# Kernel tuning notes

Hardware: AMD Instinct MI355X
Metric: run time of the kernel (lower is better)

Reference implementation:

```python
import jax, jax.numpy as jnp
import numpy as np

N_NODES = 100000
N_EDGES = 1600000
N_GRAPHS = 256
NEG_SLOPE_GAT = 0.2   # GATConv default
NEG_SLOPE_ACT = 0.01  # F.leaky_relu default


def _leaky(x, s):
    return jnp.where(x >= 0, x, s * x)


def _gat_layer(x, src, dst, W, a_src, a_dst, b, n):
    # h = W x ; per-node attention logits
    h = x @ W                      # [N, D]
    al_s = h @ a_src               # [N]
    al_d = h @ a_dst               # [N]
    e = _leaky(al_s[src] + al_d[dst], NEG_SLOPE_GAT)  # [E]
    # segment softmax over incoming edges of each dst node
    m = jax.ops.segment_max(e, dst, num_segments=n)
    m = jnp.where(jnp.isfinite(m), m, 0.0)
    ex = jnp.exp(e - m[dst])
    s = jax.ops.segment_sum(ex, dst, num_segments=n)
    alpha = ex / (s[dst] + 1e-16)
    out = jax.ops.segment_sum(h[src] * alpha[:, None], dst, num_segments=n)
    return out + b


def setup_inputs() -> dict:
    key = jax.random.key(0)
    ks = jax.random.split(key, 12)
    x = jax.random.normal(ks[0], (N_NODES, 72), dtype=jnp.float32)
    edge_index = jax.random.randint(ks[1], (2, N_EDGES), 0, N_NODES, dtype=jnp.int64)
    batch = jnp.sort(jax.random.randint(ks[2], (N_NODES,), 0, N_GRAPHS, dtype=jnp.int64))
    def glorot(k, shape):
        fan = shape[0] + shape[-1]
        return jax.random.normal(k, shape, dtype=jnp.float32) * jnp.sqrt(2.0 / fan)
    return {
        "x": x, "edge_index": edge_index, "batch": batch,
        "W1": glorot(ks[3], (72, 64)),
        "a_src1": glorot(ks[4], (64,)), "a_dst1": glorot(ks[5], (64,)),
        "b1": jnp.zeros((64,), jnp.float32),
        "W2": glorot(ks[6], (64, 64)),
        "a_src2": glorot(ks[7], (64,)), "a_dst2": glorot(ks[8], (64,)),
        "b2": jnp.zeros((64,), jnp.float32),
        "fcW": glorot(ks[9], (64, 2)),
        "fcb": jnp.zeros((2,), jnp.float32),
    }


def reference(x, edge_index, batch, W1, a_src1, a_dst1, b1, W2, a_src2, a_dst2, b2, fcW, fcb):
    n = x.shape[0]
    # PyG GATConv adds self-loops by default
    loops = jnp.arange(n, dtype=edge_index.dtype)
    src = jnp.concatenate([edge_index[0], loops])
    dst = jnp.concatenate([edge_index[1], loops])
    h = _gat_layer(x, src, dst, W1, a_src1, a_dst1, b1, n)
    h = _leaky(h, NEG_SLOPE_ACT)
    h = _gat_layer(h, src, dst, W2, a_src2, a_dst2, b2, n)
    # global mean pool over graphs
    sums = jax.ops.segment_sum(h, batch, num_segments=N_GRAPHS)
    cnt = jax.ops.segment_sum(jnp.ones((n,), h.dtype), batch, num_segments=N_GRAPHS)
    pooled = sums / jnp.maximum(cnt, 1.0)[:, None]
    # dropout is identity at inference
    return pooled @ fcW + fcb
```

## Files before the change

### kernel.cpp

```cpp
#include <hip/hip_runtime.h>
#include <hip/hip_bf16.h>
#include <math.h>


#define NPB 256
#define EPB 4096
#define PSTRIDE 4608
#define XPAD 68

__device__ __forceinline__ unsigned int f2bf(float v) {
    unsigned int b = __float_as_uint(v);
    b += 0x7FFFu + ((b >> 16) & 1u);
    return b >> 16;
}

__global__ __launch_bounds__(256) void init_all(int* __restrict__ bcur, int NB) {
    int i = blockIdx.x * 256 + threadIdx.x;
    if (i < NB) bcur[i] = 0;
}

__global__ __launch_bounds__(256) void partition(const int* __restrict__ ei,
                                                 int E, int NB,
                                                 int* __restrict__ bcur,
                                                 unsigned int* __restrict__ pairs) {
    __shared__ int h[512];
    __shared__ int hb[512];
    int t = threadIdx.x;
    for (int i = t; i < 512; i += 256) h[i] = 0;
    __syncthreads();
    int i0 = blockIdx.x * EPB;
    unsigned int val[16];
    int bk[16], r[16];
#pragma unroll
    for (int k = 0; k < 16; k++) {
        int i = i0 + k * 256 + t;
        bk[k] = -1;
        if (i < E) {
            int s = ei[i];
            int d = ei[E + i];
            bk[k] = d >> 8;
            val[k] = (unsigned)s | ((unsigned)(d & 255) << 24);
            r[k] = atomicAdd(&h[bk[k]], 1);
        }
    }
    __syncthreads();
    for (int b = t; b < NB; b += 256)
        hb[b] = h[b] ? atomicAdd(&bcur[b], h[b]) : 0;
    __syncthreads();
#pragma unroll
    for (int k = 0; k < 16; k++) {
        if (bk[k] < 0) continue;
        int pos = hb[bk[k]] + r[k];
        if (pos < PSTRIDE)
            pairs[(size_t)bk[k] * PSTRIDE + pos] = val[k];
    }
}

__global__ __launch_bounds__(256) void build_csr(const unsigned int* __restrict__ pairs,
                                                 const int* __restrict__ bcur,
                                                 int n, int NB,
                                                 int* __restrict__ rowptr,
                                                 int* __restrict__ srcs) {
    int b = blockIdx.x, t = threadIdx.x;
    __shared__ int c[512];
    __shared__ int s2[256];
    __shared__ int sbase, stot;
    int c0 = (2 * t < NB) ? min(bcur[2 * t], PSTRIDE) : 0;
    int c1 = (2 * t + 1 < NB) ? min(bcur[2 * t + 1], PSTRIDE) : 0;
    c[2 * t] = c0; c[2 * t + 1] = c1;
    s2[t] = c0 + c1;
    __syncthreads();
    for (int o = 1; o < 256; o <<= 1) {
        int u = (t >= o) ? s2[t - o] : 0;
        __syncthreads();
        s2[t] += u;
        __syncthreads();
    }
    if (t == 0) {
        int p = b >> 1;
        int ex = s2[p] - (c[2 * p] + c[2 * p + 1]);
        sbase = ex + ((b & 1) ? c[b & ~1] : 0);
        stot = s2[255];
    }
    __syncthreads();
    int d0 = b << 8;
    int nb = min(NPB, n - d0);
    int cnt_b = c[b];
    int csr0 = sbase + d0;
    const unsigned int* pb = pairs + (size_t)b * PSTRIDE;

    __shared__ int deg[NPB];
    __shared__ int cur[NPB];
    __shared__ int tmp[NPB];
    deg[t] = (t < nb) ? 1 : 0;
    __syncthreads();
    for (int j = t; j < cnt_b; j += 256)
        atomicAdd(&deg[pb[j] >> 24], 1);
    __syncthreads();
    int v = deg[t];
    tmp[t] = v;
    __syncthreads();
    for (int o = 1; o < NPB; o <<= 1) {
        int u = (t >= o) ? tmp[t - o] : 0;
        __syncthreads();
        tmp[t] += u;
        __syncthreads();
    }
    int excl = tmp[t] - v;
    if (t < nb) {
        rowptr[d0 + t] = csr0 + excl;
        srcs[csr0 + excl] = d0 + t;
        cur[t] = excl + 1;
    }
    __syncthreads();
    for (int j = t; j < cnt_b; j += 256) {
        unsigned int p = pb[j];
        int off = atomicAdd(&cur[p >> 24], 1);
        srcs[csr0 + off] = (int)(p & 0x00FFFFFFu);
    }
    if (b == 0 && t == 0) rowptr[n] = n + stot;
}

template <int IN_DIM>
__global__ __launch_bounds__(256) void node_gemm(const float* __restrict__ x,
                                                 const float* __restrict__ W,
                                                 const float* __restrict__ a_src,
                                                 const float* __restrict__ a_dst,
                                                 const float* __restrict__ bias_in,
                                                 float slope_in,
                                                 unsigned short* __restrict__ h16,
                                                 float* __restrict__ al_s,
                                                 float* __restrict__ al_d,
                                                 int n) {
    __shared__ float Ws[IN_DIM * 64];
    __shared__ float xs[IN_DIM][XPAD];
    int t = threadIdx.x;
    int nbase = blockIdx.x * 64;

    for (int idx = t; idx < IN_DIM * 16; idx += 256)
        ((float4*)Ws)[idx] = ((const float4*)W)[idx];
    const float* xb = x + (size_t)nbase * IN_DIM;
    int lim = min(64, n - nbase) * IN_DIM;
    for (int idx = t; idx < 64 * IN_DIM; idx += 256) {
        int node = idx / IN_DIM;
        int k = idx - node * IN_DIM;
        float v = 0.0f;
        if (idx < lim) {
            v = xb[idx];
            if (bias_in) {
                v += bias_in[k];
                v = (v >= 0.0f) ? v : slope_in * v;
            }
        }
        xs[k][node] = v;
    }
    __syncthreads();

    int cg = t & 15;
    int ng = t >> 4;
    float acc[4][4] = {};
#pragma unroll 8
    for (int k = 0; k < IN_DIM; k++) {
        float4 xv = *(const float4*)&xs[k][ng * 4];
        float4 wv = *(const float4*)&Ws[k * 64 + cg * 4];
        float xa[4] = {xv.x, xv.y, xv.z, xv.w};
        float wa[4] = {wv.x, wv.y, wv.z, wv.w};
#pragma unroll
        for (int i = 0; i < 4; i++)
#pragma unroll
            for (int j = 0; j < 4; j++)
                acc[i][j] += xa[i] * wa[j];
    }

    float4 as4 = *(const float4*)(a_src + cg * 4);
    float4 ad4 = *(const float4*)(a_dst + cg * 4);
#pragma unroll
    for (int i = 0; i < 4; i++) {
        int node = nbase + ng * 4 + i;
        if (node < n) {
            uint2 p;
            p.x = f2bf(acc[i][0]) | (f2bf(acc[i][1]) << 16);
            p.y = f2bf(acc[i][2]) | (f2bf(acc[i][3]) << 16);
            *(uint2*)(h16 + (size_t)node * 64 + cg * 4) = p;
        }
        float vs = acc[i][0] * as4.x + acc[i][1] * as4.y +
                   acc[i][2] * as4.z + acc[i][3] * as4.w;
        float vd = acc[i][0] * ad4.x + acc[i][1] * ad4.y +
                   acc[i][2] * ad4.z + acc[i][3] * ad4.w;
#pragma unroll
        for (int o = 8; o; o >>= 1) {
            vs += __shfl_xor(vs, o);
            vd += __shfl_xor(vd, o);
        }
        if (cg == 0 && node < n) { al_s[node] = vs; al_d[node] = vd; }
    }
}

__device__ __forceinline__ void bf8_fma(float* acc, uint4 q, float w) {
    acc[0] += w * __uint_as_float(q.x << 16);
    acc[1] += w * __uint_as_float(q.x & 0xFFFF0000u);
    acc[2] += w * __uint_as_float(q.y << 16);
    acc[3] += w * __uint_as_float(q.y & 0xFFFF0000u);
    acc[4] += w * __uint_as_float(q.z << 16);
    acc[5] += w * __uint_as_float(q.z & 0xFFFF0000u);
    acc[6] += w * __uint_as_float(q.w << 16);
    acc[7] += w * __uint_as_float(q.w & 0xFFFF0000u);
}

__global__ __launch_bounds__(256) void gat_aggregate(const int* __restrict__ rowptr,
                                                     const int* __restrict__ srcs,
                                                     const float* __restrict__ als,
                                                     const float* __restrict__ ald,
                                                     const unsigned short* __restrict__ h16,
                                                     float* __restrict__ hout,
                                                     int n) {
    int t = threadIdx.x;
    int sub = t >> 3, lane = t & 7;
    int node = blockIdx.x * 32 + sub;
    if (node >= n) return;
    int beg = rowptr[node], end = rowptr[node + 1];
    float aldv = ald[node];
    const unsigned short* hb = h16 + lane * 8;

    float acc[8] = {};
    float sm = 0.0f;
    int j = beg;
    for (; j + 4 <= end; j += 4) {
        int s0 = srcs[j], s1 = srcs[j + 1], s2 = srcs[j + 2], s3 = srcs[j + 3];
        float e0 = als[s0] + aldv, e1 = als[s1] + aldv;
        float e2 = als[s2] + aldv, e3 = als[s3] + aldv;
        uint4 q0 = *(const uint4*)(hb + (size_t)s0 * 64);
        uint4 q1 = *(const uint4*)(hb + (size_t)s1 * 64);
        uint4 q2 = *(const uint4*)(hb + (size_t)s2 * 64);
        uint4 q3 = *(const uint4*)(hb + (size_t)s3 * 64);
        e0 = (e0 >= 0.0f) ? e0 : 0.2f * e0;
        e1 = (e1 >= 0.0f) ? e1 : 0.2f * e1;
        e2 = (e2 >= 0.0f) ? e2 : 0.2f * e2;
        e3 = (e3 >= 0.0f) ? e3 : 0.2f * e3;
        float w0 = __expf(e0), w1 = __expf(e1);
        float w2 = __expf(e2), w3 = __expf(e3);
        sm += (w0 + w1) + (w2 + w3);
        bf8_fma(acc, q0, w0);
        bf8_fma(acc, q1, w1);
        bf8_fma(acc, q2, w2);
        bf8_fma(acc, q3, w3);
    }
    for (; j < end; j++) {
        int s = srcs[j];
        float e = als[s] + aldv;
        e = (e >= 0.0f) ? e : 0.2f * e;
        float w = __expf(e);
        uint4 q = *(const uint4*)(hb + (size_t)s * 64);
        sm += w;
        bf8_fma(acc, q, w);
    }

    float inv = 1.0f / (sm + 1e-16f);
    float4 o0 = make_float4(acc[0] * inv, acc[1] * inv, acc[2] * inv, acc[3] * inv);
    float4 o1 = make_float4(acc[4] * inv, acc[5] * inv, acc[6] * inv, acc[7] * inv);
    float* op = hout + (size_t)node * 64 + lane * 8;
    *(float4*)op = o0;
    *(float4*)(op + 4) = o1;
}

__global__ __launch_bounds__(256) void pool_fc(const float* __restrict__ hout,
                                               const float* __restrict__ b2,
                                               const int* __restrict__ batch,
                                               const float* __restrict__ fcW,
                                               const float* __restrict__ fcb,
                                               float* __restrict__ out, int n) {
    int g = blockIdx.x;
    int t = threadIdx.x;
    __shared__ int sLo, sHi;
    __shared__ float red[4][64];
    if (t == 0) {
        int lo = 0, hi = n;
        while (lo < hi) { int m = (lo + hi) >> 1; if (batch[m] < g) lo = m + 1; else hi = m; }
        sLo = lo;
    } else if (t == 64) {
        int lo = 0, hi = n;
        while (lo < hi) { int m = (lo + hi) >> 1; if (batch[m] < g + 1) lo = m + 1; else hi = m; }
        sHi = lo;
    }
    __syncthreads();
    int lo = sLo, hi = sHi;
    int wv = t >> 6, lane = t & 63;
    float acc = 0.0f;
    for (int node = lo + wv; node < hi; node += 4)
        acc += hout[(size_t)node * 64 + lane];
    red[wv][lane] = acc;
    __syncthreads();
    if (wv == 0) {
        float c = (float)(hi - lo);
        float s = red[0][lane] + red[1][lane] + red[2][lane] + red[3][lane];
        s += c * b2[lane];
        float cd = (c > 1.0f) ? c : 1.0f;
        float p = s / cd;
        float s0 = p * fcW[lane * 2 + 0];
        float s1 = p * fcW[lane * 2 + 1];
#pragma unroll
        for (int o = 32; o; o >>= 1) {
            s0 += __shfl_xor(s0, o);
            s1 += __shfl_xor(s1, o);
        }
        if (lane == 0) {
            out[g * 2 + 0] = s0 + fcb[0];
            out[g * 2 + 1] = s1 + fcb[1];
        }
    }
}

extern "C" void kernel_launch(void* const* d_in, const int* in_sizes, int n_in,
                              void* d_out, int out_size, void* d_ws, size_t ws_size,
                              hipStream_t stream) {
    const float* x    = (const float*)d_in[0];
    const int*   ei   = (const int*)d_in[1];
    const int*   batch= (const int*)d_in[2];
    const float* W1   = (const float*)d_in[3];
    const float* as1  = (const float*)d_in[4];
    const float* ad1  = (const float*)d_in[5];
    const float* b1   = (const float*)d_in[6];
    const float* W2   = (const float*)d_in[7];
    const float* as2  = (const float*)d_in[8];
    const float* ad2  = (const float*)d_in[9];
    const float* b2   = (const float*)d_in[10];
    const float* fcW  = (const float*)d_in[11];
    const float* fcb  = (const float*)d_in[12];
    float* out = (float*)d_out;

    const int N = in_sizes[2];
    const int E = in_sizes[1] / 2;
    const int G = out_size / 2;
    const int tot = E + N;
    const int NB = (N + NPB - 1) / NPB;

    float* ws     = (float*)d_ws;
    float* bufO   = ws;
    unsigned int* pairs = (unsigned int*)(bufO + (size_t)N * 64);
    float* als    = (float*)(pairs + (size_t)NB * PSTRIDE);
    float* ald    = als + N;
    int*   rowptr = (int*)(ald + N);
    int*   srcs   = rowptr + N + 1;
    int*   bcur   = srcs + tot;
    unsigned short* bufH16 = (unsigned short*)(bcur + NB);

    dim3 b256(256);
    int gInit = (NB + 255) / 256;
    int gPart = (E + EPB - 1) / EPB;
    int gGemm = (N + 63) / 64;
    int gAgg  = (N + 31) / 32;

    init_all<<<gInit, b256, 0, stream>>>(bcur, NB);
    partition<<<gPart, b256, 0, stream>>>(ei, E, NB, bcur, pairs);
    build_csr<<<NB, b256, 0, stream>>>(pairs, bcur, N, NB, rowptr, srcs);

    node_gemm<72><<<gGemm, b256, 0, stream>>>(x, W1, as1, ad1, nullptr, 0.0f,
                                              bufH16, als, ald, N);
    gat_aggregate<<<gAgg, b256, 0, stream>>>(rowptr, srcs, als, ald, bufH16, bufO, N);

    node_gemm<64><<<gGemm, b256, 0, stream>>>(bufO, W2, as2, ad2, b1, 0.01f,
                                              bufH16, als, ald, N);
    gat_aggregate<<<gAgg, b256, 0, stream>>>(rowptr, srcs, als, ald, bufH16, bufO, N);

    pool_fc<<<G, b256, 0, stream>>>(bufO, b2, batch, fcW, fcb, out, N);
}
```

Baseline: 336.3 us.

## Sort CSR edges by source bucket, prefetch aggregate indices, alias pairs buffer

In build_csr, each block now runs a counting sort of its edge pairs into shared memory, keyed on the high bits of the source index, before the degree and scatter passes. This orders each node's source list by source locality, which should improve cache hits on h16 and als gathers in the aggregate kernels. The aggregate loop now software-prefetches the next four source indices to hide index-load latency. The pairs buffer is aliased onto bufO to shrink the workspace. The sort adds about 18KB of shared memory and an extra pass, which may lower build_csr occupancy.

Measured after the change: 331.0 us. About the same (-1.6%).

```diff
diff --git a/kernel.cpp b/kernel.cpp
--- a/kernel.cpp
+++ b/kernel.cpp
@@ -65,10 +65,14 @@
     __shared__ int c[512];
     __shared__ int s2[256];
     __shared__ int sbase, stot;
+    __shared__ unsigned int Q[PSTRIDE];
+    __shared__ int hist[256];
+    __shared__ int hcur[256];
     int c0 = (2 * t < NB) ? min(bcur[2 * t], PSTRIDE) : 0;
     int c1 = (2 * t + 1 < NB) ? min(bcur[2 * t + 1], PSTRIDE) : 0;
     c[2 * t] = c0; c[2 * t + 1] = c1;
     s2[t] = c0 + c1;
+    hist[t] = 0;
     __syncthreads();
     for (int o = 1; o < 256; o <<= 1) {
         int u = (t >= o) ? s2[t - o] : 0;
@@ -89,13 +93,34 @@
     int csr0 = sbase + d0;
     const unsigned int* pb = pairs + (size_t)b * PSTRIDE;
 
+    for (int j = t; j < cnt_b; j += 256)
+        atomicAdd(&hist[(pb[j] & 0xFFFFFFu) >> 9], 1);
+    __syncthreads();
+    int hv = hist[t];
+    hcur[t] = hv;
+    __syncthreads();
+    for (int o = 1; o < 256; o <<= 1) {
+        int u = (t >= o) ? hcur[t - o] : 0;
+        __syncthreads();
+        hcur[t] += u;
+        __syncthreads();
+    }
+    hcur[t] -= hv;
+    __syncthreads();
+    for (int j = t; j < cnt_b; j += 256) {
+        unsigned int p = pb[j];
+        int pos = atomicAdd(&hcur[(p & 0xFFFFFFu) >> 9], 1);
+        Q[pos] = p;
+    }
+    __syncthreads();
+
     __shared__ int deg[NPB];
     __shared__ int cur[NPB];
     __shared__ int tmp[NPB];
     deg[t] = (t < nb) ? 1 : 0;
     __syncthreads();
     for (int j = t; j < cnt_b; j += 256)
-        atomicAdd(&deg[pb[j] >> 24], 1);
+        atomicAdd(&deg[Q[j] >> 24], 1);
     __syncthreads();
     int v = deg[t];
     tmp[t] = v;
@@ -114,7 +139,7 @@
     }
     __syncthreads();
     for (int j = t; j < cnt_b; j += 256) {
-        unsigned int p = pb[j];
+        unsigned int p = Q[j];
         int off = atomicAdd(&cur[p >> 24], 1);
         srcs[csr0 + off] = (int)(p & 0x00FFFFFFu);
     }
@@ -225,25 +250,50 @@
     float acc[8] = {};
     float sm = 0.0f;
     int j = beg;
-    for (; j + 4 <= end; j += 4) {
+    if (j + 4 <= end) {
         int s0 = srcs[j], s1 = srcs[j + 1], s2 = srcs[j + 2], s3 = srcs[j + 3];
-        float e0 = als[s0] + aldv, e1 = als[s1] + aldv;
-        float e2 = als[s2] + aldv, e3 = als[s3] + aldv;
-        uint4 q0 = *(const uint4*)(hb + (size_t)s0 * 64);
-        uint4 q1 = *(const uint4*)(hb + (size_t)s1 * 64);
-        uint4 q2 = *(const uint4*)(hb + (size_t)s2 * 64);
-        uint4 q3 = *(const uint4*)(hb + (size_t)s3 * 64);
-        e0 = (e0 >= 0.0f) ? e0 : 0.2f * e0;
-        e1 = (e1 >= 0.0f) ? e1 : 0.2f * e1;
-        e2 = (e2 >= 0.0f) ? e2 : 0.2f * e2;
-        e3 = (e3 >= 0.0f) ? e3 : 0.2f * e3;
-        float w0 = __expf(e0), w1 = __expf(e1);
-        float w2 = __expf(e2), w3 = __expf(e3);
-        sm += (w0 + w1) + (w2 + w3);
-        bf8_fma(acc, q0, w0);
-        bf8_fma(acc, q1, w1);
-        bf8_fma(acc, q2, w2);
-        bf8_fma(acc, q3, w3);
+        for (; j + 8 <= end; j += 4) {
+            int n0 = srcs[j + 4], n1 = srcs[j + 5];
+            int n2 = srcs[j + 6], n3 = srcs[j + 7];
+            float e0 = als[s0] + aldv, e1 = als[s1] + aldv;
+            float e2 = als[s2] + aldv, e3 = als[s3] + aldv;
+            uint4 q0 = *(const uint4*)(hb + (size_t)s0 * 64);
+            uint4 q1 = *(const uint4*)(hb + (size_t)s1 * 64);
+            uint4 q2 = *(const uint4*)(hb + (size_t)s2 * 64);
+            uint4 q3 = *(const uint4*)(hb + (size_t)s3 * 64);
+            e0 = (e0 >= 0.0f) ? e0 : 0.2f * e0;
+            e1 = (e1 >= 0.0f) ? e1 : 0.2f * e1;
+            e2 = (e2 >= 0.0f) ? e2 : 0.2f * e2;
+            e3 = (e3 >= 0.0f) ? e3 : 0.2f * e3;
+            float w0 = __expf(e0), w1 = __expf(e1);
+            float w2 = __expf(e2), w3 = __expf(e3);
+            sm += (w0 + w1) + (w2 + w3);
+            bf8_fma(acc, q0, w0);
+            bf8_fma(acc, q1, w1);
+            bf8_fma(acc, q2, w2);
+            bf8_fma(acc, q3, w3);
+            s0 = n0; s1 = n1; s2 = n2; s3 = n3;
+        }
+        {
+            float e0 = als[s0] + aldv, e1 = als[s1] + aldv;
+            float e2 = als[s2] + aldv, e3 = als[s3] + aldv;
+            uint4 q0 = *(const uint4*)(hb + (size_t)s0 * 64);
+            uint4 q1 = *(const uint4*)(hb + (size_t)s1 * 64);
+            uint4 q2 = *(const uint4*)(hb + (size_t)s2 * 64);
+            uint4 q3 = *(const uint4*)(hb + (size_t)s3 * 64);
+            e0 = (e0 >= 0.0f) ? e0 : 0.2f * e0;
+            e1 = (e1 >= 0.0f) ? e1 : 0.2f * e1;
+            e2 = (e2 >= 0.0f) ? e2 : 0.2f * e2;
+            e3 = (e3 >= 0.0f) ? e3 : 0.2f * e3;
+            float w0 = __expf(e0), w1 = __expf(e1);
+            float w2 = __expf(e2), w3 = __expf(e3);
+            sm += (w0 + w1) + (w2 + w3);
+            bf8_fma(acc, q0, w0);
+            bf8_fma(acc, q1, w1);
+            bf8_fma(acc, q2, w2);
+            bf8_fma(acc, q3, w3);
+            j += 4;
+        }
     }
     for (; j < end; j++) {
         int s = srcs[j];
@@ -336,8 +386,8 @@
 
     float* ws     = (float*)d_ws;
     float* bufO   = ws;
-    unsigned int* pairs = (unsigned int*)(bufO + (size_t)N * 64);
-    float* als    = (float*)(pairs + (size_t)NB * PSTRIDE);
+    unsigned int* pairs  = (unsigned int*)bufO;
+    float* als    = bufO + (size_t)N * 64;
     float* ald    = als + N;
     int*   rowptr = (int*)(ald + N);
     int*   srcs   = rowptr + N + 1;
```
